# Kernel tuning notes

Hardware: AMD Instinct MI355X
Metric: run time of the kernel (lower is better)

## Reference

```python
import jax, jax.numpy as jnp
import numpy as np

EPS = 1e-9


def _squash(s, axis=-1):
    # squash(s) = (|s|^2 / (1+|s|^2)) * s / |s|
    sq = jnp.sum(jnp.square(s), axis=axis, keepdims=True)
    norm = jnp.sqrt(sq + EPS)
    return (sq / (1.0 + sq)) * (s / norm)


def setup_inputs() -> dict:
    key = jax.random.key(0)
    B, N_IN, N_OUT, ATOMS = 32, 2048, 64, 16
    votes = jax.random.normal(key, (B, N_IN, N_OUT, ATOMS), dtype=jnp.float32)
    return {"votes": votes, "num_routing": 3}


def reference(votes, num_routing):
    # votes: [B, in_caps, out_caps, atoms]
    temper = 1.0
    softmax_in = False
    B, n_in, n_out, atoms = votes.shape
    logits = jnp.zeros((B, n_in, n_out, 1), dtype=votes.dtype)
    pose = None
    for i in range(num_routing):
        # coupling coefficients: softmax over out-caps axis (softmax_in=False)
        ax = 1 if softmax_in else 2
        c = jax.nn.softmax(logits * temper, axis=ax)  # [B, in, out, 1]
        # weighted pooling over input capsules -> [B, 1, out, atoms]
        preact = jnp.sum(c * votes, axis=1, keepdims=True)
        pose = _squash(preact, axis=-1)
        if i < num_routing - 1:
            # agreement: <votes, pose> over atoms -> [B, in, out, 1]
            logits = logits + jnp.sum(votes * pose, axis=-1, keepdims=True)
    prob = jnp.sqrt(jnp.sum(jnp.square(pose), axis=-1, keepdims=True) + EPS)  # [B,1,out,1]
    pose_out = jnp.squeeze(pose, axis=-3)          # [B, out, atoms]
    prob_out = jnp.squeeze(prob, axis=(-3, -1))    # [B, out]
    return pose_out, prob_out
```

## Files before the change

### kernel.cpp

```cpp
#include <hip/hip_runtime.h>


#define NB 32
#define NIN 2048
#define NOUT 64
#define ATOMS 16
#define EPSF 1e-9f

#define ROWS_PER_WAVE 8
#define WAVES_PER_BLOCK 4
#define ROWS_PER_BLOCK (ROWS_PER_WAVE * WAVES_PER_BLOCK)
#define CHUNKS (NIN / ROWS_PER_BLOCK)
#define RBATCH 2

template <int USE_POSE>
__global__ __launch_bounds__(256, 4) void route_pass(
    const float4* __restrict__ votes4,
    const float4* __restrict__ pose_accum4,
    float4* __restrict__ partials4)
{
    const int b     = blockIdx.x / CHUNKS;
    const int chunk = blockIdx.x % CHUNKS;
    const int wave  = threadIdx.x >> 6;
    const int lane  = threadIdx.x & 63;

    float4 pse[4];
    if (USE_POSE) {
#pragma unroll
        for (int j = 0; j < 4; ++j)
            pse[j] = pose_accum4[(b * NOUT + j * 16 + (lane >> 2)) * 4 + (lane & 3)];
    }

    float4 acc[4];
#pragma unroll
    for (int j = 0; j < 4; ++j) acc[j] = make_float4(0.f, 0.f, 0.f, 0.f);

    const int in0 = chunk * ROWS_PER_BLOCK + wave * ROWS_PER_WAVE;
    const float4* vrow = votes4 + (size_t)(b * NIN + in0) * 256 + lane;

    for (int r0 = 0; r0 < ROWS_PER_WAVE; r0 += RBATCH) {
        float4 v[RBATCH][4];
#pragma unroll
        for (int r = 0; r < RBATCH; ++r) {
            const float4* vp = vrow + (size_t)(r0 + r) * 256;
#pragma unroll
            for (int j = 0; j < 4; ++j) v[r][j] = vp[j * 64];
        }

        if (USE_POSE) {
            float lg[RBATCH][4];
#pragma unroll
            for (int r = 0; r < RBATCH; ++r)
#pragma unroll
                for (int j = 0; j < 4; ++j) {
                    float d = v[r][j].x * pse[j].x;
                    d = fmaf(v[r][j].y, pse[j].y, d);
                    d = fmaf(v[r][j].z, pse[j].z, d);
                    d = fmaf(v[r][j].w, pse[j].w, d);
                    lg[r][j] = d;
                }
#pragma unroll
            for (int mask = 1; mask <= 2; mask <<= 1)
#pragma unroll
                for (int r = 0; r < RBATCH; ++r)
#pragma unroll
                    for (int j = 0; j < 4; ++j)
                        lg[r][j] += __shfl_xor(lg[r][j], mask, 64);

            float e[RBATCH][4], s[RBATCH];
#pragma unroll
            for (int r = 0; r < RBATCH; ++r) {
                float t = 0.f;
#pragma unroll
                for (int j = 0; j < 4; ++j) { e[r][j] = __expf(lg[r][j]); t += e[r][j]; }
                s[r] = t;
            }
#pragma unroll
            for (int mask = 4; mask <= 32; mask <<= 1)
#pragma unroll
                for (int r = 0; r < RBATCH; ++r)
                    s[r] += __shfl_xor(s[r], mask, 64);

#pragma unroll
            for (int r = 0; r < RBATCH; ++r) {
                float inv = __frcp_rn(s[r]);
#pragma unroll
                for (int j = 0; j < 4; ++j) {
                    float c = e[r][j] * inv;
                    acc[j].x = fmaf(c, v[r][j].x, acc[j].x);
                    acc[j].y = fmaf(c, v[r][j].y, acc[j].y);
                    acc[j].z = fmaf(c, v[r][j].z, acc[j].z);
                    acc[j].w = fmaf(c, v[r][j].w, acc[j].w);
                }
            }
        } else {
#pragma unroll
            for (int r = 0; r < RBATCH; ++r)
#pragma unroll
                for (int j = 0; j < 4; ++j) {
                    acc[j].x += v[r][j].x; acc[j].y += v[r][j].y;
                    acc[j].z += v[r][j].z; acc[j].w += v[r][j].w;
                }
        }
    }
    if (!USE_POSE) {
#pragma unroll
        for (int j = 0; j < 4; ++j) {
            acc[j].x *= (1.f / 64.f); acc[j].y *= (1.f / 64.f);
            acc[j].z *= (1.f / 64.f); acc[j].w *= (1.f / 64.f);
        }
    }

    __shared__ float4 red4[WAVES_PER_BLOCK * 256];
#pragma unroll
    for (int j = 0; j < 4; ++j)
        red4[wave * 256 + j * 64 + lane] = acc[j];
    __syncthreads();

    float4* pblock4 = partials4 + ((size_t)(b * CHUNKS + chunk) << 8);
    {
        int idx = threadIdx.x;
        float4 a = red4[idx], b2 = red4[256 + idx], c = red4[512 + idx], d = red4[768 + idx];
        float4 t;
        t.x = (a.x + b2.x) + (c.x + d.x);
        t.y = (a.y + b2.y) + (c.y + d.y);
        t.z = (a.z + b2.z) + (c.z + d.z);
        t.w = (a.w + b2.w) + (c.w + d.w);
        pblock4[idx] = t;
    }
}

__global__ __launch_bounds__(256) void squash_reduce(
    const float* __restrict__ partials,
    float* __restrict__ pose_accum,
    float* __restrict__ d_out,
    int mode)
{
    int gid = blockIdx.x * 256 + threadIdx.x;
    int b  = gid >> 10;
    int oa = gid & 1023;
    const float* p = partials + ((size_t)b << 16) + oa;
    float s0 = 0.f, s1 = 0.f, s2 = 0.f, s3 = 0.f;
#pragma unroll
    for (int c = 0; c < CHUNKS; c += 4) {
        s0 += p[(c + 0) << 10];
        s1 += p[(c + 1) << 10];
        s2 += p[(c + 2) << 10];
        s3 += p[(c + 3) << 10];
    }
    float s = (s0 + s1) + (s2 + s3);

    float sq = s * s;
#pragma unroll
    for (int mask = 1; mask < ATOMS; mask <<= 1)
        sq += __shfl_xor(sq, mask, 64);
    float norm = sqrtf(sq + EPSF);
    float f = (sq / (1.0f + sq)) / norm;
    float pse = f * s;
    if (mode == 0) {
        pose_accum[gid] = pse;
    } else if (mode == 1) {
        pose_accum[gid] += pse;
    } else {
        d_out[gid] = pse;
        if ((gid & (ATOMS - 1)) == 0) {
            float psq = f * f * sq;
            d_out[NB * NOUT * ATOMS + (gid >> 4)] = sqrtf(psq + EPSF);
        }
    }
}

extern "C" void kernel_launch(void* const* d_in, const int* in_sizes, int n_in,
                              void* d_out, int out_size, void* d_ws, size_t ws_size,
                              hipStream_t stream) {
    const float4* votes4 = (const float4*)d_in[0];
    float* out = (float*)d_out;

    float* pose_accum = (float*)d_ws;
    float* partials   = pose_accum + NB * NOUT * ATOMS;

    dim3 blk(256);
    dim3 grid_route(NB * CHUNKS);
    dim3 grid_sq(NB * NOUT * ATOMS / 256);

    route_pass<0><<<grid_route, blk, 0, stream>>>(votes4, nullptr, (float4*)partials);
    squash_reduce<<<grid_sq, blk, 0, stream>>>(partials, pose_accum, nullptr, 0);

    route_pass<1><<<grid_route, blk, 0, stream>>>(votes4, (const float4*)pose_accum, (float4*)partials);
    squash_reduce<<<grid_sq, blk, 0, stream>>>(partials, pose_accum, nullptr, 1);

    route_pass<1><<<grid_route, blk, 0, stream>>>(votes4, (const float4*)pose_accum, (float4*)partials);
    squash_reduce<<<grid_sq, blk, 0, stream>>>(partials, nullptr, out, 2);
}
```

Baseline: 446.7 us.

## Transcode votes to fp16 in first pass and route later passes on half data

The first routing pass now also writes an fp16 copy of the votes into workspace, and later pose-weighted passes read the half-precision copy with a new lane mapping (8 atoms per lane). This cuts the bytes read in the two bandwidth-bound agreement passes roughly in half, at the cost of an extra write in pass one and reduced precision of votes. It falls back to the fp32 path if the workspace is too small.

```diff
diff --git a/kernel.cpp b/kernel.cpp
--- a/kernel.cpp
+++ b/kernel.cpp
@@ -1,4 +1,5 @@
 #include <hip/hip_runtime.h>
+#include <hip/hip_fp16.h>
 
 
 #define NB 32
@@ -13,8 +14,185 @@
 #define CHUNKS (NIN / ROWS_PER_BLOCK)
 #define RBATCH 2
 
-template <int USE_POSE>
-__global__ __launch_bounds__(256, 4) void route_pass(
+__device__ __forceinline__ float4 f4add(float4 a, float4 b) {
+    return make_float4(a.x + b.x, a.y + b.y, a.z + b.z, a.w + b.w);
+}
+__device__ __forceinline__ float4 f4fma(float c, float4 v, float4 a) {
+    return make_float4(fmaf(c, v.x, a.x), fmaf(c, v.y, a.y),
+                       fmaf(c, v.z, a.z), fmaf(c, v.w, a.w));
+}
+__device__ __forceinline__ float f4dot(float4 a, float4 b) {
+    float d = a.x * b.x;
+    d = fmaf(a.y, b.y, d); d = fmaf(a.z, b.z, d); d = fmaf(a.w, b.w, d);
+    return d;
+}
+
+template <int TRANSCODE>
+__global__ __launch_bounds__(256, 4) void route0_transcode(
+    const float4* __restrict__ votes4,
+    uint2* __restrict__ votesh,
+    float4* __restrict__ partials4)
+{
+    const int b     = blockIdx.x / CHUNKS;
+    const int chunk = blockIdx.x % CHUNKS;
+    const int wave  = threadIdx.x >> 6;
+    const int lane  = threadIdx.x & 63;
+
+    float4 acc[4];
+#pragma unroll
+    for (int j = 0; j < 4; ++j) acc[j] = make_float4(0.f, 0.f, 0.f, 0.f);
+
+    const int in0 = chunk * ROWS_PER_BLOCK + wave * ROWS_PER_WAVE;
+    const float4* vrow = votes4 + (size_t)(b * NIN + in0) * 256 + lane;
+    uint2* hrow = votesh + (size_t)(b * NIN + in0) * 256 + lane;
+
+    for (int r0 = 0; r0 < ROWS_PER_WAVE; r0 += RBATCH) {
+        float4 v[RBATCH][4];
+#pragma unroll
+        for (int r = 0; r < RBATCH; ++r) {
+            const float4* vp = vrow + (size_t)(r0 + r) * 256;
+#pragma unroll
+            for (int j = 0; j < 4; ++j) v[r][j] = vp[j * 64];
+        }
+#pragma unroll
+        for (int r = 0; r < RBATCH; ++r) {
+#pragma unroll
+            for (int j = 0; j < 4; ++j) {
+                acc[j] = f4add(acc[j], v[r][j]);
+                if (TRANSCODE) {
+                    __half2 h01 = __floats2half2_rn(v[r][j].x, v[r][j].y);
+                    __half2 h23 = __floats2half2_rn(v[r][j].z, v[r][j].w);
+                    uint2 pk;
+                    pk.x = *(const unsigned int*)&h01;
+                    pk.y = *(const unsigned int*)&h23;
+                    (hrow + (size_t)(r0 + r) * 256)[j * 64] = pk;
+                }
+            }
+        }
+    }
+#pragma unroll
+    for (int j = 0; j < 4; ++j) {
+        acc[j].x *= (1.f / 64.f); acc[j].y *= (1.f / 64.f);
+        acc[j].z *= (1.f / 64.f); acc[j].w *= (1.f / 64.f);
+    }
+
+    __shared__ float4 red4[WAVES_PER_BLOCK * 256];
+#pragma unroll
+    for (int j = 0; j < 4; ++j)
+        red4[wave * 256 + j * 64 + lane] = acc[j];
+    __syncthreads();
+
+    float4* pblock4 = partials4 + ((size_t)(b * CHUNKS + chunk) << 8);
+    {
+        int idx = threadIdx.x;
+        float4 a = red4[idx], b2 = red4[256 + idx], c = red4[512 + idx], d = red4[768 + idx];
+        float4 t;
+        t.x = (a.x + b2.x) + (c.x + d.x);
+        t.y = (a.y + b2.y) + (c.y + d.y);
+        t.z = (a.z + b2.z) + (c.z + d.z);
+        t.w = (a.w + b2.w) + (c.w + d.w);
+        pblock4[idx] = t;
+    }
+}
+
+__global__ __launch_bounds__(256, 4) void route_pose_fp16(
+    const uint4* __restrict__ voteshv,
+    const float4* __restrict__ pose_accum4,
+    float4* __restrict__ partials4)
+{
+    const int b     = blockIdx.x / CHUNKS;
+    const int chunk = blockIdx.x % CHUNKS;
+    const int wave  = threadIdx.x >> 6;
+    const int lane  = threadIdx.x & 63;
+
+    float4 pseh[2][2];
+#pragma unroll
+    for (int j = 0; j < 2; ++j)
+#pragma unroll
+        for (int h = 0; h < 2; ++h)
+            pseh[j][h] = pose_accum4[(size_t)b * 256
+                                     + (j * 32 + (lane >> 1)) * 4 + (lane & 1) * 2 + h];
+
+    float4 acc[2][2];
+#pragma unroll
+    for (int j = 0; j < 2; ++j)
+#pragma unroll
+        for (int h = 0; h < 2; ++h) acc[j][h] = make_float4(0.f, 0.f, 0.f, 0.f);
+
+    const int in0 = chunk * ROWS_PER_BLOCK + wave * ROWS_PER_WAVE;
+    const uint4* vrow = voteshv + (size_t)(b * NIN + in0) * 128 + lane;
+
+    for (int r0 = 0; r0 < ROWS_PER_WAVE; r0 += RBATCH) {
+        float4 va[RBATCH][2][2];
+        float lg[RBATCH][2];
+#pragma unroll
+        for (int r = 0; r < RBATCH; ++r) {
+#pragma unroll
+            for (int j = 0; j < 2; ++j) {
+                uint4 q = vrow[(size_t)(r0 + r) * 128 + j * 64];
+                float2 f0 = __half22float2(*(const __half2*)&q.x);
+                float2 f1 = __half22float2(*(const __half2*)&q.y);
+                float2 f2 = __half22float2(*(const __half2*)&q.z);
+                float2 f3 = __half22float2(*(const __half2*)&q.w);
+                va[r][j][0] = make_float4(f0.x, f0.y, f1.x, f1.y);
+                va[r][j][1] = make_float4(f2.x, f2.y, f3.x, f3.y);
+                lg[r][j] = f4dot(va[r][j][0], pseh[j][0]) +
+                           f4dot(va[r][j][1], pseh[j][1]);
+            }
+        }
+#pragma unroll
+        for (int r = 0; r < RBATCH; ++r)
+#pragma unroll
+            for (int j = 0; j < 2; ++j)
+                lg[r][j] += __shfl_xor(lg[r][j], 1, 64);
+
+        float e[RBATCH][2], s[RBATCH];
+#pragma unroll
+        for (int r = 0; r < RBATCH; ++r) {
+            e[r][0] = __expf(lg[r][0]);
+            e[r][1] = __expf(lg[r][1]);
+            s[r] = e[r][0] + e[r][1];
+        }
+#pragma unroll
+        for (int mask = 2; mask <= 32; mask <<= 1)
+#pragma unroll
+            for (int r = 0; r < RBATCH; ++r)
+                s[r] += __shfl_xor(s[r], mask, 64);
+
+#pragma unroll
+        for (int r = 0; r < RBATCH; ++r) {
+            float inv = __frcp_rn(s[r]);
+#pragma unroll
+            for (int j = 0; j < 2; ++j) {
+                float c = e[r][j] * inv;
+                acc[j][0] = f4fma(c, va[r][j][0], acc[j][0]);
+                acc[j][1] = f4fma(c, va[r][j][1], acc[j][1]);
+            }
+        }
+    }
+
+    __shared__ float4 red4[WAVES_PER_BLOCK * 256];
+#pragma unroll
+    for (int j = 0; j < 2; ++j)
+#pragma unroll
+        for (int h = 0; h < 2; ++h)
+            red4[wave * 256 + j * 128 + (lane >> 1) * 4 + (lane & 1) * 2 + h] = acc[j][h];
+    __syncthreads();
+
+    float4* pblock4 = partials4 + ((size_t)(b * CHUNKS + chunk) << 8);
+    {
+        int idx = threadIdx.x;
+        float4 a = red4[idx], b2 = red4[256 + idx], c = red4[512 + idx], d = red4[768 + idx];
+        float4 t;
+        t.x = (a.x + b2.x) + (c.x + d.x);
+        t.y = (a.y + b2.y) + (c.y + d.y);
+        t.z = (a.z + b2.z) + (c.z + d.z);
+        t.w = (a.w + b2.w) + (c.w + d.w);
+        pblock4[idx] = t;
+    }
+}
+
+__global__ __launch_bounds__(256, 4) void route_pose_fp32(
     const float4* __restrict__ votes4,
     const float4* __restrict__ pose_accum4,
     float4* __restrict__ partials4)
@@ -25,11 +203,9 @@
     const int lane  = threadIdx.x & 63;
 
     float4 pse[4];
-    if (USE_POSE) {
-#pragma unroll
-        for (int j = 0; j < 4; ++j)
-            pse[j] = pose_accum4[(b * NOUT + j * 16 + (lane >> 2)) * 4 + (lane & 3)];
-    }
+#pragma unroll
+    for (int j = 0; j < 4; ++j)
+        pse[j] = pose_accum4[(b * NOUT + j * 16 + (lane >> 2)) * 4 + (lane & 3)];
 
     float4 acc[4];
 #pragma unroll
@@ -40,74 +216,44 @@
 
     for (int r0 = 0; r0 < ROWS_PER_WAVE; r0 += RBATCH) {
         float4 v[RBATCH][4];
+        float lg[RBATCH][4];
 #pragma unroll
         for (int r = 0; r < RBATCH; ++r) {
             const float4* vp = vrow + (size_t)(r0 + r) * 256;
 #pragma unroll
-            for (int j = 0; j < 4; ++j) v[r][j] = vp[j * 64];
-        }
-
-        if (USE_POSE) {
-            float lg[RBATCH][4];
+            for (int j = 0; j < 4; ++j) {
+                v[r][j] = vp[j * 64];
+                lg[r][j] = f4dot(v[r][j], pse[j]);
+            }
+        }
+#pragma unroll
+        for (int mask = 1; mask <= 2; mask <<= 1)
 #pragma unroll
             for (int r = 0; r < RBATCH; ++r)
 #pragma unroll
-                for (int j = 0; j < 4; ++j) {
-                    float d = v[r][j].x * pse[j].x;
-                    d = fmaf(v[r][j].y, pse[j].y, d);
-                    d = fmaf(v[r][j].z, pse[j].z, d);
-                    d = fmaf(v[r][j].w, pse[j].w, d);
-                    lg[r][j] = d;
-                }
-#pragma unroll
-            for (int mask = 1; mask <= 2; mask <<= 1)
-#pragma unroll
-                for (int r = 0; r < RBATCH; ++r)
-#pragma unroll
-                    for (int j = 0; j < 4; ++j)
-                        lg[r][j] += __shfl_xor(lg[r][j], mask, 64);
-
-            float e[RBATCH][4], s[RBATCH];
-#pragma unroll
-            for (int r = 0; r < RBATCH; ++r) {
-                float t = 0.f;
-#pragma unroll
-                for (int j = 0; j < 4; ++j) { e[r][j] = __expf(lg[r][j]); t += e[r][j]; }
-                s[r] = t;
-            }
-#pragma unroll
-            for (int mask = 4; mask <= 32; mask <<= 1)
-#pragma unroll
-                for (int r = 0; r < RBATCH; ++r)
-                    s[r] += __shfl_xor(s[r], mask, 64);
-
-#pragma unroll
-            for (int r = 0; r < RBATCH; ++r) {
-                float inv = __frcp_rn(s[r]);
-#pragma unroll
-                for (int j = 0; j < 4; ++j) {
-                    float c = e[r][j] * inv;
-                    acc[j].x = fmaf(c, v[r][j].x, acc[j].x);
-                    acc[j].y = fmaf(c, v[r][j].y, acc[j].y);
-                    acc[j].z = fmaf(c, v[r][j].z, acc[j].z);
-                    acc[j].w = fmaf(c, v[r][j].w, acc[j].w);
-                }
-            }
-        } else {
+                for (int j = 0; j < 4; ++j)
+                    lg[r][j] += __shfl_xor(lg[r][j], mask, 64);
+
+        float e[RBATCH][4], s[RBATCH];
+#pragma unroll
+        for (int r = 0; r < RBATCH; ++r) {
+            float t = 0.f;
+#pragma unroll
+            for (int j = 0; j < 4; ++j) { e[r][j] = __expf(lg[r][j]); t += e[r][j]; }
+            s[r] = t;
+        }
+#pragma unroll
+        for (int mask = 4; mask <= 32; mask <<= 1)
 #pragma unroll
             for (int r = 0; r < RBATCH; ++r)
-#pragma unroll
-                for (int j = 0; j < 4; ++j) {
-                    acc[j].x += v[r][j].x; acc[j].y += v[r][j].y;
-                    acc[j].z += v[r][j].z; acc[j].w += v[r][j].w;
-                }
-        }
-    }
-    if (!USE_POSE) {
-#pragma unroll
-        for (int j = 0; j < 4; ++j) {
-            acc[j].x *= (1.f / 64.f); acc[j].y *= (1.f / 64.f);
-            acc[j].z *= (1.f / 64.f); acc[j].w *= (1.f / 64.f);
+                s[r] += __shfl_xor(s[r], mask, 64);
+
+#pragma unroll
+        for (int r = 0; r < RBATCH; ++r) {
+            float inv = __frcp_rn(s[r]);
+#pragma unroll
+            for (int j = 0; j < 4; ++j)
+                acc[j] = f4fma(e[r][j] * inv, v[r][j], acc[j]);
         }
     }
 
@@ -178,17 +324,41 @@
 
     float* pose_accum = (float*)d_ws;
     float* partials   = pose_accum + NB * NOUT * ATOMS;
+    uint2* votesh     = (uint2*)(partials + NB * CHUNKS * 1024);
+    const size_t need_fp16 =
+        ((size_t)NB * NOUT * ATOMS + (size_t)NB * CHUNKS * 1024) * sizeof(float)
+        + (size_t)NB * NIN * NOUT * ATOMS * sizeof(__half);
 
     dim3 blk(256);
     dim3 grid_route(NB * CHUNKS);
     dim3 grid_sq(NB * NOUT * ATOMS / 256);
 
-    route_pass<0><<<grid_route, blk, 0, stream>>>(votes4, nullptr, (float4*)partials);
+    const bool fp16_path = (ws_size >= need_fp16);
+
+    if (fp16_path) {
+        route0_transcode<1><<<grid_route, blk, 0, stream>>>(
+            votes4, votesh, (float4*)partials);
+    } else {
+        route0_transcode<0><<<grid_route, blk, 0, stream>>>(
+            votes4, nullptr, (float4*)partials);
+    }
     squash_reduce<<<grid_sq, blk, 0, stream>>>(partials, pose_accum, nullptr, 0);
 
-    route_pass<1><<<grid_route, blk, 0, stream>>>(votes4, (const float4*)pose_accum, (float4*)partials);
+    if (fp16_path) {
+        route_pose_fp16<<<grid_route, blk, 0, stream>>>(
+            (const uint4*)votesh, (const float4*)pose_accum, (float4*)partials);
+    } else {
+        route_pose_fp32<<<grid_route, blk, 0, stream>>>(
+            votes4, (const float4*)pose_accum, (float4*)partials);
+    }
     squash_reduce<<<grid_sq, blk, 0, stream>>>(partials, pose_accum, nullptr, 1);
 
-    route_pass<1><<<grid_route, blk, 0, stream>>>(votes4, (const float4*)pose_accum, (float4*)partials);
+    if (fp16_path) {
+        route_pose_fp16<<<grid_route, blk, 0, stream>>>(
+            (const uint4*)votesh, (const float4*)pose_accum, (float4*)partials);
+    } else {
+        route_pose_fp32<<<grid_route, blk, 0, stream>>>(
+            votes4, (const float4*)pose_accum, (float4*)partials);
+    }
     squash_reduce<<<grid_sq, blk, 0, stream>>>(partials, nullptr, out, 2);
 }
```

Result: slower. 488.0 us (+9.2%).

## Stream vote rows through double-buffered LDS via async global-to-LDS loads

Applied to the files above, without the earlier changes.

Replaces the register-based batched row loads with per-wave double-buffered LDS staging using global_load_lds, waiting on vmcnt so the next row's fetch overlaps the current row's compute. The templated pass is split into two specialised kernels, and the staging buffer is reused for the cross-wave reduction. The goal is to hide memory latency in this bandwidth-bound streaming pass. In exchange it adds LDS traffic and occupancy pressure, and relies on the inline vmcnt waits being correct.

```diff
diff --git a/kernel.cpp b/kernel.cpp
--- a/kernel.cpp
+++ b/kernel.cpp
@@ -11,116 +11,176 @@
 #define WAVES_PER_BLOCK 4
 #define ROWS_PER_BLOCK (ROWS_PER_WAVE * WAVES_PER_BLOCK)
 #define CHUNKS (NIN / ROWS_PER_BLOCK)
-#define RBATCH 2
-
-template <int USE_POSE>
-__global__ __launch_bounds__(256, 4) void route_pass(
+
+__device__ __forceinline__ float4 f4add(float4 a, float4 b) {
+    return make_float4(a.x + b.x, a.y + b.y, a.z + b.z, a.w + b.w);
+}
+__device__ __forceinline__ float4 f4fma(float c, float4 v, float4 a) {
+    return make_float4(fmaf(c, v.x, a.x), fmaf(c, v.y, a.y),
+                       fmaf(c, v.z, a.z), fmaf(c, v.w, a.w));
+}
+__device__ __forceinline__ float f4dot(float4 a, float4 b) {
+    float d = a.x * b.x;
+    d = fmaf(a.y, b.y, d); d = fmaf(a.z, b.z, d); d = fmaf(a.w, b.w, d);
+    return d;
+}
+
+__device__ __forceinline__ void gload_lds16(const void* g, void* l) {
+    __builtin_amdgcn_global_load_lds(
+        (const __attribute__((address_space(1))) void*)g,
+        (__attribute__((address_space(3))) void*)l, 16, 0, 0);
+}
+
+__device__ __forceinline__ void stage_row(
+    const char* vbase_lane, float4* wstage, int r, int buf)
+{
+#pragma unroll
+    for (int q = 0; q < 4; ++q)
+        gload_lds16(vbase_lane + (size_t)r * 4096 + q * 1024,
+                    wstage + buf * 256 + q * 64);
+}
+
+__device__ __forceinline__ void wait_vm4() {
+    asm volatile("s_waitcnt vmcnt(4)" ::: "memory");
+    __builtin_amdgcn_sched_barrier(0);
+}
+__device__ __forceinline__ void wait_vm0() {
+    asm volatile("s_waitcnt vmcnt(0)" ::: "memory");
+    __builtin_amdgcn_sched_barrier(0);
+}
+
+__global__ __launch_bounds__(256, 4) void route0_lds(
     const float4* __restrict__ votes4,
-    const float4* __restrict__ pose_accum4,
     float4* __restrict__ partials4)
 {
+    __shared__ float4 stage4[WAVES_PER_BLOCK * 2 * 256];
     const int b     = blockIdx.x / CHUNKS;
     const int chunk = blockIdx.x % CHUNKS;
     const int wave  = threadIdx.x >> 6;
     const int lane  = threadIdx.x & 63;
-
-    float4 pse[4];
-    if (USE_POSE) {
+    const int in0   = chunk * ROWS_PER_BLOCK + wave * ROWS_PER_WAVE;
+
+    const char* vbase = (const char*)(votes4 + (size_t)(b * NIN + in0) * 256)
+                        + lane * 16;
+    float4* wstage = stage4 + wave * 512;
+
+    stage_row(vbase, wstage, 0, 0);
+
+    float4 acc[4];
+#pragma unroll
+    for (int j = 0; j < 4; ++j) acc[j] = make_float4(0.f, 0.f, 0.f, 0.f);
+
+    for (int r = 0; r < ROWS_PER_WAVE; ++r) {
+        if (r + 1 < ROWS_PER_WAVE) {
+            stage_row(vbase, wstage, r + 1, (r + 1) & 1);
+            wait_vm4();
+        } else {
+            wait_vm0();
+        }
+        const float4* vb = wstage + (r & 1) * 256 + lane;
 #pragma unroll
         for (int j = 0; j < 4; ++j)
-            pse[j] = pose_accum4[(b * NOUT + j * 16 + (lane >> 2)) * 4 + (lane & 3)];
-    }
-
-    float4 acc[4];
-#pragma unroll
-    for (int j = 0; j < 4; ++j) acc[j] = make_float4(0.f, 0.f, 0.f, 0.f);
-
-    const int in0 = chunk * ROWS_PER_BLOCK + wave * ROWS_PER_WAVE;
-    const float4* vrow = votes4 + (size_t)(b * NIN + in0) * 256 + lane;
-
-    for (int r0 = 0; r0 < ROWS_PER_WAVE; r0 += RBATCH) {
-        float4 v[RBATCH][4];
-#pragma unroll
-        for (int r = 0; r < RBATCH; ++r) {
-            const float4* vp = vrow + (size_t)(r0 + r) * 256;
-#pragma unroll
-            for (int j = 0; j < 4; ++j) v[r][j] = vp[j * 64];
-        }
-
-        if (USE_POSE) {
-            float lg[RBATCH][4];
-#pragma unroll
-            for (int r = 0; r < RBATCH; ++r)
-#pragma unroll
-                for (int j = 0; j < 4; ++j) {
-                    float d = v[r][j].x * pse[j].x;
-                    d = fmaf(v[r][j].y, pse[j].y, d);
-                    d = fmaf(v[r][j].z, pse[j].z, d);
-                    d = fmaf(v[r][j].w, pse[j].w, d);
-                    lg[r][j] = d;
-                }
-#pragma unroll
-            for (int mask = 1; mask <= 2; mask <<= 1)
-#pragma unroll
-                for (int r = 0; r < RBATCH; ++r)
-#pragma unroll
-                    for (int j = 0; j < 4; ++j)
-                        lg[r][j] += __shfl_xor(lg[r][j], mask, 64);
-
-            float e[RBATCH][4], s[RBATCH];
-#pragma unroll
-            for (int r = 0; r < RBATCH; ++r) {
-                float t = 0.f;
-#pragma unroll
-                for (int j = 0; j < 4; ++j) { e[r][j] = __expf(lg[r][j]); t += e[r][j]; }
-                s[r] = t;
-            }
-#pragma unroll
-            for (int mask = 4; mask <= 32; mask <<= 1)
-#pragma unroll
-                for (int r = 0; r < RBATCH; ++r)
-                    s[r] += __shfl_xor(s[r], mask, 64);
-
-#pragma unroll
-            for (int r = 0; r < RBATCH; ++r) {
-                float inv = __frcp_rn(s[r]);
-#pragma unroll
-                for (int j = 0; j < 4; ++j) {
-                    float c = e[r][j] * inv;
-                    acc[j].x = fmaf(c, v[r][j].x, acc[j].x);
-                    acc[j].y = fmaf(c, v[r][j].y, acc[j].y);
-                    acc[j].z = fmaf(c, v[r][j].z, acc[j].z);
-                    acc[j].w = fmaf(c, v[r][j].w, acc[j].w);
-                }
-            }
-        } else {
-#pragma unroll
-            for (int r = 0; r < RBATCH; ++r)
-#pragma unroll
-                for (int j = 0; j < 4; ++j) {
-                    acc[j].x += v[r][j].x; acc[j].y += v[r][j].y;
-                    acc[j].z += v[r][j].z; acc[j].w += v[r][j].w;
-                }
-        }
-    }
-    if (!USE_POSE) {
-#pragma unroll
-        for (int j = 0; j < 4; ++j) {
-            acc[j].x *= (1.f / 64.f); acc[j].y *= (1.f / 64.f);
-            acc[j].z *= (1.f / 64.f); acc[j].w *= (1.f / 64.f);
-        }
-    }
-
-    __shared__ float4 red4[WAVES_PER_BLOCK * 256];
+            acc[j] = f4add(acc[j], vb[j * 64]);
+    }
+#pragma unroll
+    for (int j = 0; j < 4; ++j) {
+        acc[j].x *= (1.f / 64.f); acc[j].y *= (1.f / 64.f);
+        acc[j].z *= (1.f / 64.f); acc[j].w *= (1.f / 64.f);
+    }
+
+    __syncthreads();
 #pragma unroll
     for (int j = 0; j < 4; ++j)
-        red4[wave * 256 + j * 64 + lane] = acc[j];
+        stage4[wave * 256 + j * 64 + lane] = acc[j];
     __syncthreads();
 
     float4* pblock4 = partials4 + ((size_t)(b * CHUNKS + chunk) << 8);
     {
         int idx = threadIdx.x;
-        float4 a = red4[idx], b2 = red4[256 + idx], c = red4[512 + idx], d = red4[768 + idx];
+        float4 a = stage4[idx], b2 = stage4[256 + idx],
+               c = stage4[512 + idx], d = stage4[768 + idx];
+        float4 t;
+        t.x = (a.x + b2.x) + (c.x + d.x);
+        t.y = (a.y + b2.y) + (c.y + d.y);
+        t.z = (a.z + b2.z) + (c.z + d.z);
+        t.w = (a.w + b2.w) + (c.w + d.w);
+        pblock4[idx] = t;
+    }
+}
+
+__global__ __launch_bounds__(256, 4) void route_pose_lds(
+    const float4* __restrict__ votes4,
+    const float4* __restrict__ pose_accum4,
+    float4* __restrict__ partials4)
+{
+    __shared__ float4 stage4[WAVES_PER_BLOCK * 2 * 256];
+    const int b     = blockIdx.x / CHUNKS;
+    const int chunk = blockIdx.x % CHUNKS;
+    const int wave  = threadIdx.x >> 6;
+    const int lane  = threadIdx.x & 63;
+    const int in0   = chunk * ROWS_PER_BLOCK + wave * ROWS_PER_WAVE;
+
+    float4 pse[4];
+#pragma unroll
+    for (int j = 0; j < 4; ++j)
+        pse[j] = pose_accum4[(b * NOUT + j * 16 + (lane >> 2)) * 4 + (lane & 3)];
+
+    const char* vbase = (const char*)(votes4 + (size_t)(b * NIN + in0) * 256)
+                        + lane * 16;
+    float4* wstage = stage4 + wave * 512;
+
+    stage_row(vbase, wstage, 0, 0);
+
+    float4 acc[4];
+#pragma unroll
+    for (int j = 0; j < 4; ++j) acc[j] = make_float4(0.f, 0.f, 0.f, 0.f);
+
+    for (int r = 0; r < ROWS_PER_WAVE; ++r) {
+        if (r + 1 < ROWS_PER_WAVE) {
+            stage_row(vbase, wstage, r + 1, (r + 1) & 1);
+            wait_vm4();
+        } else {
+            wait_vm0();
+        }
+        const float4* vb = wstage + (r & 1) * 256 + lane;
+
+        float4 v[4];
+        float lg[4];
+#pragma unroll
+        for (int j = 0; j < 4; ++j) {
+            v[j] = vb[j * 64];
+            lg[j] = f4dot(v[j], pse[j]);
+        }
+#pragma unroll
+        for (int mask = 1; mask <= 2; mask <<= 1)
+#pragma unroll
+            for (int j = 0; j < 4; ++j)
+                lg[j] += __shfl_xor(lg[j], mask, 64);
+
+        float e[4], s = 0.f;
+#pragma unroll
+        for (int j = 0; j < 4; ++j) { e[j] = __expf(lg[j]); s += e[j]; }
+#pragma unroll
+        for (int mask = 4; mask <= 32; mask <<= 1)
+            s += __shfl_xor(s, mask, 64);
+
+        float inv = __frcp_rn(s);
+#pragma unroll
+        for (int j = 0; j < 4; ++j)
+            acc[j] = f4fma(e[j] * inv, v[j], acc[j]);
+    }
+
+    __syncthreads();
+#pragma unroll
+    for (int j = 0; j < 4; ++j)
+        stage4[wave * 256 + j * 64 + lane] = acc[j];
+    __syncthreads();
+
+    float4* pblock4 = partials4 + ((size_t)(b * CHUNKS + chunk) << 8);
+    {
+        int idx = threadIdx.x;
+        float4 a = stage4[idx], b2 = stage4[256 + idx],
+               c = stage4[512 + idx], d = stage4[768 + idx];
         float4 t;
         t.x = (a.x + b2.x) + (c.x + d.x);
         t.y = (a.y + b2.y) + (c.y + d.y);
@@ -183,12 +243,14 @@
     dim3 grid_route(NB * CHUNKS);
     dim3 grid_sq(NB * NOUT * ATOMS / 256);
 
-    route_pass<0><<<grid_route, blk, 0, stream>>>(votes4, nullptr, (float4*)partials);
+    route0_lds<<<grid_route, blk, 0, stream>>>(votes4, (float4*)partials);
     squash_reduce<<<grid_sq, blk, 0, stream>>>(partials, pose_accum, nullptr, 0);
 
-    route_pass<1><<<grid_route, blk, 0, stream>>>(votes4, (const float4*)pose_accum, (float4*)partials);
+    route_pose_lds<<<grid_route, blk, 0, stream>>>(
+        votes4, (const float4*)pose_accum, (float4*)partials);
     squash_reduce<<<grid_sq, blk, 0, stream>>>(partials, pose_accum, nullptr, 1);
 
-    route_pass<1><<<grid_route, blk, 0, stream>>>(votes4, (const float4*)pose_accum, (float4*)partials);
+    route_pose_lds<<<grid_route, blk, 0, stream>>>(
+        votes4, (const float4*)pose_accum, (float4*)partials);
     squash_reduce<<<grid_sq, blk, 0, stream>>>(partials, nullptr, out, 2);
 }
```

Measured after the change: 524.5 us. +17.4%, slower.
